# Kernel tuning notes

Hardware: AMD Instinct MI355X
Metric: run time of the kernel (lower is better)

Reference implementation:

```python
import jax, jax.numpy as jnp
import numpy as np

MAX_SEGMENTS = 196
BN_EPS = 1e-5

def _conv(x, w, pad, dil=1):
    return jax.lax.conv_general_dilated(
        x, w, window_strides=(1, 1), padding=[(pad, pad), (pad, pad)],
        rhs_dilation=(dil, dil), dimension_numbers=('NCHW', 'OIHW', 'NCHW'))

def _bn(x, g, b, m, v):
    inv = g / jnp.sqrt(v + BN_EPS)
    return x * inv[None, :, None, None] + (b - m * inv)[None, :, None, None]

def setup_inputs() -> dict:
    key = jax.random.key(0)
    ks = jax.random.split(key, 20)
    B, H, W = 2, 224, 224
    E = 768
    inp = {
        'img': jax.random.normal(ks[0], (B, 3, H, W), jnp.float32),
        'segments': jax.random.randint(ks[1], (B, H, W), 0, MAX_SEGMENTS, jnp.int32),
        'centroids': jax.random.uniform(ks[2], (B, MAX_SEGMENTS, 2), jnp.float32) * 223.0,
        'conv1_w': jax.random.normal(ks[3], (64, 3, 3, 3), jnp.float32) * 0.1,
        'conv1_b': jax.random.normal(ks[4], (64,), jnp.float32) * 0.1,
        'bn1_g': jax.random.uniform(ks[5], (64,), jnp.float32) + 0.5,
        'bn1_b': jax.random.normal(ks[6], (64,), jnp.float32) * 0.1,
        'bn1_m': jax.random.normal(ks[7], (64,), jnp.float32) * 0.1,
        'bn1_v': jax.random.uniform(ks[8], (64,), jnp.float32) + 0.5,
        'conv2_w': jax.random.normal(ks[9], (E, 64, 3, 3), jnp.float32) * 0.05,
        'conv2_b': jax.random.normal(ks[10], (E,), jnp.float32) * 0.1,
        'bn2_g': jax.random.uniform(ks[11], (E,), jnp.float32) + 0.5,
        'bn2_b': jax.random.normal(ks[12], (E,), jnp.float32) * 0.1,
        'bn2_m': jax.random.normal(ks[13], (E,), jnp.float32) * 0.1,
        'bn2_v': jax.random.uniform(ks[14], (E,), jnp.float32) + 0.5,
        'edge_w': jax.random.normal(ks[15], (2, 1, 3, 3), jnp.float32) * 0.2,
        'pos_w': jax.random.normal(ks[16], (E, 2), jnp.float32) * 0.5,
        'pos_b': jax.random.normal(ks[17], (E,), jnp.float32) * 0.1,
        'fusion_w': jax.random.normal(ks[18], (E, 2 * E), jnp.float32) * 0.02,
        'fusion_b': jax.random.normal(ks[19], (E,), jnp.float32) * 0.1,
    }
    return inp

def reference(img, segments, centroids, conv1_w, conv1_b, bn1_g, bn1_b, bn1_m, bn1_v,
              conv2_w, conv2_b, bn2_g, bn2_b, bn2_m, bn2_v, edge_w,
              pos_w, pos_b, fusion_w, fusion_b):
    B, _, H, W = img.shape
    M = MAX_SEGMENTS
    # CNN feature extractor: [B, E, H, W]
    x = jax.nn.relu(_bn(_conv(img, conv1_w, pad=1) + conv1_b[None, :, None, None],
                        bn1_g, bn1_b, bn1_m, bn1_v))
    feats = jax.nn.relu(_bn(_conv(x, conv2_w, pad=2, dil=2) + conv2_b[None, :, None, None],
                            bn2_g, bn2_b, bn2_m, bn2_v))
    C = feats.shape[1]
    # Edge detection on grayscale
    gray = jnp.mean(img, axis=1, keepdims=True)
    edges = _conv(gray, edge_w, pad=1)  # [B, 2, H, W]
    gradient_map = jnp.sqrt(edges[:, 0] ** 2 + edges[:, 1] ** 2 + 1e-8)  # [B, H, W]
    similarity = jnp.clip(1.0 - gradient_map, 0.0, 1.0)
    # Global per-(batch, segment) ids
    ids = (jnp.arange(B, dtype=jnp.int32)[:, None] * M + segments.reshape(B, -1)).reshape(-1)
    K = B * M
    ones = jnp.ones((B * H * W,), jnp.float32)
    counts = jax.ops.segment_sum(ones, ids, num_segments=K)              # [K]
    n_K = jnp.maximum(counts, 1.0)
    sim_sum = jax.ops.segment_sum(similarity.reshape(-1), ids, num_segments=K)
    W_k = (sim_sum / n_K).reshape(B, M)
    # Segment mean / max pooling of features
    ff = feats.transpose(0, 2, 3, 1).reshape(-1, C)                      # [B*H*W, C]
    emb_mean = (jax.ops.segment_sum(ff, ids, num_segments=K) / n_K[:, None]).reshape(B, M, C)
    mx = jax.ops.segment_max(ff, ids, num_segments=K)
    emb_max = jnp.where(counts[:, None] > 0, mx, 0.0).reshape(B, M, C)   # empty segments -> 0
    concat = jnp.concatenate([emb_mean, emb_max], axis=-1)               # [B, M, 2C]
    fused = jnp.einsum('bmc,dc->bmd', concat, fusion_w) + fusion_b
    weighted = fused * W_k[:, :, None]
    # Positional embeddings from normalized centroids
    cn = jnp.stack([centroids[:, :, 0] / float(W), centroids[:, :, 1] / float(H)], axis=-1)
    pos = jnp.einsum('bmc,dc->bmd', cn, pos_w) + pos_b                   # n_centroids == M
    final_embeddings = weighted + pos
    return final_embeddings, gradient_map, segments
```

## Files before the change

kernel.cpp:

```cpp
#include <hip/hip_runtime.h>
#include <hip/hip_fp8.h>

#define B_ 2
#define H_ 224
#define W_ 224
#define HW_ 50176
#define E_ 768
#define M_ 196

typedef __attribute__((ext_vector_type(8))) short short8;
typedef __attribute__((ext_vector_type(8))) unsigned short ushort8;
typedef __attribute__((ext_vector_type(4))) float floatx4;

__device__ __forceinline__ float bf2f(ushort u){ return __uint_as_float(((unsigned)u)<<16); }
__device__ __forceinline__ ushort f2bf(float f){
  unsigned b = __float_as_uint(f);
  b += 0x7fffu + ((b>>16)&1u);
  return (ushort)(b>>16);
}
__device__ __forceinline__ unsigned pack4_fp8(float a, float b, float c, float d){
  int v = __builtin_amdgcn_cvt_pk_fp8_f32(a, b, 0, false);
  v = __builtin_amdgcn_cvt_pk_fp8_f32(c, d, v, true);
  return (unsigned)v;
}

__global__ void prep_edge_k(const float* __restrict__ w2, const float* __restrict__ cb2,
                            const float* __restrict__ g2, const float* __restrict__ be2,
                            const float* __restrict__ mn2, const float* __restrict__ vr2,
                            ushort* __restrict__ wt2, float* __restrict__ bias2,
                            const float* __restrict__ w1, const float* __restrict__ cb1,
                            const float* __restrict__ g1, const float* __restrict__ be1,
                            const float* __restrict__ mn1, const float* __restrict__ vr1,
                            ushort* __restrict__ wA, float* __restrict__ bias1,
                            const float* __restrict__ img, const int* __restrict__ seg,
                            const float* __restrict__ ew, float* __restrict__ out,
                            float* __restrict__ counts, float* __restrict__ sims,
                            int* __restrict__ scnt){
  __shared__ ushort WT[9216];
  __shared__ float aux[196];
  __shared__ float aux2[196];
  int tid = threadIdx.x;
  if (blockIdx.x < 48){
    int co0 = blockIdx.x * 16;
    if (tid < 16){
      float inv = g2[co0+tid] * rsqrtf(vr2[co0+tid] + 1e-5f);
      aux[tid] = inv;
      bias2[co0+tid] = cb2[co0+tid]*inv + be2[co0+tid] - mn2[co0+tid]*inv;
    }
    __syncthreads();
    #pragma unroll
    for (int j = 0; j < 36; j++){
      int idx = j*256 + tid;
      WT[idx] = f2bf(w2[(size_t)co0*576 + idx] * aux[idx/576]);
    }
    __syncthreads();
    #pragma unroll
    for (int j = 0; j < 5; j++){
      int o = j*256 + tid;
      if (o < 1152){
        int tapkc = o >> 4, col = o & 15;
        int tap = tapkc >> 3, kc = tapkc & 7;
        ushort tmp[8];
        #pragma unroll
        for (int e=0; e<8; e++)
          tmp[e] = WT[col*576 + (kc*8+e)*9 + tap];
        *reinterpret_cast<uint4*>(&wt2[(size_t)((tap*8 + kc)*768 + co0 + col)*8]) =
            *reinterpret_cast<const uint4*>(tmp);
      }
    }
    return;
  }
  if (blockIdx.x == 48){
    #pragma unroll
    for (int j = 0; j < 8; j++){
      int t = j*256 + tid;
      int co = t >> 5, k = t & 31;
      float inv = g1[co] * rsqrtf(vr1[co] + 1e-5f);
      float val = 0.f;
      if (k < 27){
        int tap = k / 3, ci = k % 3;
        val = w1[co*27 + ci*9 + tap] * inv;
      }
      wA[co*32 + k] = f2bf(val);
      if (k == 0) bias1[co] = cb1[co]*inv + be1[co] - mn1[co]*inv;
    }
    return;
  }
  if (tid < 196){ aux[tid]=0.f; aux2[tid]=0.f; }
  __syncthreads();
  int p = (blockIdx.x-49)*256 + tid;
  int b = p / HW_; int r = p % HW_; int h = r / W_; int w = r % W_;
  float e0=0.f, e1=0.f;
  #pragma unroll
  for (int ky=0;ky<3;ky++){
    int hh=h+ky-1;
    #pragma unroll
    for (int kx=0;kx<3;kx++){
      int ww=w+kx-1;
      float gv=0.f;
      if (hh>=0&&hh<H_&&ww>=0&&ww<W_){
        int base = b*3*HW_ + hh*W_ + ww;
        gv=(img[base]+img[base+HW_]+img[base+2*HW_])*(1.f/3.f);
      }
      e0 += gv*ew[ky*3+kx];
      e1 += gv*ew[9+ky*3+kx];
    }
  }
  float gm = sqrtf(e0*e0+e1*e1+1e-8f);
  out[301056 + p] = gm;
  int sg = seg[p];
  out[401408 + p] = (float)sg;
  float sim = fminf(fmaxf(1.f-gm,0.f),1.f);
  atomicAdd(&aux[sg], 1.f);
  atomicAdd(&aux2[sg], sim);
  __syncthreads();
  if (tid < 196){
    int gid = b*196 + tid;
    float c = aux[tid];
    atomicAdd(&counts[gid], c);
    atomicAdd(&sims[gid], aux2[tid]);
    atomicAdd(&scnt[b*196+tid], (int)c);
  }
}

__launch_bounds__(256)
__global__ void conv1_scan_k(const float* __restrict__ img, const ushort* __restrict__ wA,
                             const float* __restrict__ bias1, ushort* __restrict__ xbf,
                             const int* __restrict__ scnt, int* __restrict__ offs,
                             int* __restrict__ curs){
  __shared__ float HL[3*18*20];
  __shared__ ushort IC[256*40];
  __shared__ ushort AW[64*40];
  __shared__ float b1s[64];
  int tid = threadIdx.x;
  if (blockIdx.x < 2){
    int* a = reinterpret_cast<int*>(HL);
    int s = blockIdx.x;
    a[tid] = (tid<196)? scnt[s*196+tid] : 0;
    __syncthreads();
    for (int d=1; d<256; d<<=1){
      int v = a[tid];
      int u = (tid>=d)? a[tid-d] : 0;
      __syncthreads();
      a[tid] = v+u;
      __syncthreads();
    }
    if (tid<=196) offs[s*200+tid] = tid ? a[tid-1] : 0;
    if (tid<196)  curs[s*196+tid] = tid ? a[tid-1] : 0;
    return;
  }
  int bid = blockIdx.x - 2;
  int b = bid / 196, tile = bid % 196;
  int tr = tile / 14, tc = tile % 14;
  int h0 = tr*16, w0 = tc*16;
  for (int idx = tid; idx < 972; idx += 256){
    int ci = idx / 324, rem = idx % 324;
    int r = rem / 18, c = rem % 18;
    int hh = h0 + r - 1, ww = w0 + c - 1;
    float v = (hh>=0 && hh<H_ && ww>=0 && ww<W_) ? img[((b*3+ci)*H_+hh)*W_+ww] : 0.f;
    HL[ci*360 + r*20 + c] = v;
  }
  {
    int row = tid >> 2, cp = (tid&3)*8;
    uint4 v = *reinterpret_cast<const uint4*>(&wA[row*32 + cp]);
    *reinterpret_cast<uint4*>(&AW[row*40 + cp]) = v;
  }
  if (tid < 64) b1s[tid] = bias1[tid];
  __syncthreads();
  {
    int pr = tid >> 4, pc = tid & 15;
    ushort tmp[32];
    #pragma unroll
    for (int ky=0; ky<3; ky++)
      #pragma unroll
      for (int kx=0; kx<3; kx++)
        #pragma unroll
        for (int ci=0; ci<3; ci++)
          tmp[(ky*3+kx)*3+ci] = f2bf(HL[ci*360 + (pr+ky)*20 + (pc+kx)]);
    #pragma unroll
    for (int k=27; k<32; k++) tmp[k] = 0;
    #pragma unroll
    for (int j=0; j<4; j++)
      *reinterpret_cast<uint4*>(&IC[tid*40 + j*8]) = *reinterpret_cast<const uint4*>(&tmp[j*8]);
  }
  __syncthreads();
  int lane = tid & 63, wave = tid >> 6;
  int q = lane >> 4, l15 = lane & 15;
  short8 af[4], bfr[4];
  #pragma unroll
  for (int f=0; f<4; f++)
    af[f] = *reinterpret_cast<const short8*>(&AW[(f*16+l15)*40 + q*8]);
  #pragma unroll
  for (int f=0; f<4; f++)
    bfr[f] = *reinterpret_cast<const short8*>(&IC[(wave*64+f*16+l15)*40 + q*8]);
  floatx4 acc[4][4];
  #pragma unroll
  for (int fc=0; fc<4; fc++)
    #pragma unroll
    for (int fp=0; fp<4; fp++){
      floatx4 z = (floatx4){0.f,0.f,0.f,0.f};
      acc[fc][fp] = __builtin_amdgcn_mfma_f32_16x16x32_bf16(af[fc], bfr[fp], z, 0,0,0);
    }
  #pragma unroll
  for (int fp=0; fp<4; fp++){
    int pxl = wave*64 + fp*16 + l15;
    size_t gp = (size_t)b*HW_ + (size_t)(h0 + (pxl>>4))*W_ + (w0 + (pxl&15));
    #pragma unroll
    for (int fc=0; fc<4; fc++){
      int co4 = fc*16 + q*4;
      ushort o[4];
      #pragma unroll
      for (int r=0; r<4; r++) o[r] = f2bf(fmaxf(acc[fc][fp][r] + b1s[co4+r], 0.f));
      *reinterpret_cast<uint2*>(&xbf[gp*64 + co4]) = *reinterpret_cast<const uint2*>(o);
    }
  }
}

__launch_bounds__(256, 2)
__global__ void conv2_scatter_k(const ushort* __restrict__ xbf, const ushort* __restrict__ wt2,
                                const float* __restrict__ bias2, unsigned char* __restrict__ feats,
                                const int* __restrict__ seg, int* __restrict__ curs,
                                int* __restrict__ list){
  __shared__ ushort SM[25600];
  ushort* XH = SM;
  int tid = threadIdx.x;
  if (blockIdx.y == 0){
    if (blockIdx.x < 392){
      int p = blockIdx.x*256 + tid;
      int b = p / HW_;
      int pos = atomicAdd(&curs[b*196+seg[p]], 1);
      list[b*HW_ + pos] = p;
    }
    return;
  }
  int lane = tid & 63, wave = tid >> 6;
  int wc = wave >> 1, wp = wave & 1;
  int q = lane >> 4, l15 = lane & 15;
  int bt = blockIdx.x / 196, tile = blockIdx.x % 196;
  int tr = tile / 14, tc = tile % 14;
  int co0 = (blockIdx.y - 1) * 128;
  int h0 = tr*16, w0 = tc*16;

  for (int px = tid; px < 400; px += 256){
    int hr = px / 20, wcol = px % 20;
    int hh = h0 + hr - 2, ww = w0 + wcol - 2;
    bool ok = (hh>=0 && hh<H_ && ww>=0 && ww<W_);
    const uint4* src = reinterpret_cast<const uint4*>(&xbf[(((size_t)bt*H_+hh)*W_+ww)*64]);
    #pragma unroll
    for (int chl=0; chl<8; chl++){
      uint4 val = ok ? src[chl] : make_uint4(0u,0u,0u,0u);
      *reinterpret_cast<uint4*>(&XH[chl*3200 + px*8]) = val;
    }
  }
  __syncthreads();

  floatx4 acc[4][8];
  #pragma unroll
  for (int i=0;i<4;i++)
    #pragma unroll
    for (int j=0;j<8;j++) acc[i][j] = (floatx4){0.f,0.f,0.f,0.f};

  const int xb = q*3200 + wp*1280 + l15*8;
  const ushort* wgl = wt2 + ((size_t)q*768 + (size_t)(co0 + wc*64 + l15))*8;

  short8 af[2][4], bxA[4], bxB[4];
  #pragma unroll
  for (int f=0; f<4; f++)
    af[0][f] = *reinterpret_cast<const short8*>(&wgl[f*128]);
  #pragma unroll
  for (int fp=0; fp<4; fp++)
    bxA[fp] = *reinterpret_cast<const short8*>(&XH[xb + fp*160]);

  #pragma unroll
  for (int hs = 0; hs < 18; hs++){
    const int cur = hs & 1, nxt = cur ^ 1;
    const int tap = hs >> 1, half = hs & 1;
    const int dyr = (tap/3)*2, dxr = (tap%3)*2;
    const int xoff = half*12800 + dyr*160 + dxr*8;
    if (hs < 17){
      #pragma unroll
      for (int f=0; f<4; f++)
        af[nxt][f] = *reinterpret_cast<const short8*>(&wgl[(size_t)(hs+1)*24576 + f*128]);
    }
    #pragma unroll
    for (int fp=0; fp<4; fp++)
      bxB[fp] = *reinterpret_cast<const short8*>(&XH[xb + xoff + (4+fp)*160]);
    __builtin_amdgcn_sched_barrier(0);
    __builtin_amdgcn_s_setprio(1);
    #pragma unroll
    for (int fc=0; fc<4; fc++)
      #pragma unroll
      for (int fp=0; fp<4; fp++)
        acc[fc][fp] = __builtin_amdgcn_mfma_f32_16x16x32_bf16(af[cur][fc], bxA[fp],
                                                              acc[fc][fp], 0,0,0);
    __builtin_amdgcn_s_setprio(0);
    if (hs < 17){
      const int nh = hs + 1;
      const int ntap = nh >> 1, nhalf = nh & 1;
      const int nxoff = nhalf*12800 + ((ntap/3)*2)*160 + ((ntap%3)*2)*8;
      #pragma unroll
      for (int fp=0; fp<4; fp++)
        bxA[fp] = *reinterpret_cast<const short8*>(&XH[xb + nxoff + fp*160]);
    }
    __builtin_amdgcn_sched_barrier(0);
    __builtin_amdgcn_s_setprio(1);
    #pragma unroll
    for (int fc=0; fc<4; fc++)
      #pragma unroll
      for (int fp=0; fp<4; fp++)
        acc[fc][4+fp] = __builtin_amdgcn_mfma_f32_16x16x32_bf16(af[cur][fc], bxB[fp],
                                                                acc[fc][4+fp], 0,0,0);
    __builtin_amdgcn_s_setprio(0);
  }

  __syncthreads();
  unsigned* EP = reinterpret_cast<unsigned*>(SM);
  #pragma unroll
  for (int fc=0; fc<4; fc++){
    float4 bs = *reinterpret_cast<const float4*>(&bias2[co0 + wc*64 + fc*16 + q*4]);
    int cslot = wc*16 + fc*4 + q;
    #pragma unroll
    for (int fp=0; fp<8; fp++){
      int p_local = (wp*8 + fp)*16 + l15;
      EP[p_local*34 + cslot] = pack4_fp8(
          fmaxf(acc[fc][fp][0] + bs.x, 0.f), fmaxf(acc[fc][fp][1] + bs.y, 0.f),
          fmaxf(acc[fc][fp][2] + bs.z, 0.f), fmaxf(acc[fc][fp][3] + bs.w, 0.f));
    }
  }
  __syncthreads();
  {
    size_t gbase = ((size_t)bt*HW_ + (size_t)(tr*16)*W_ + tc*16)*768 + co0;
    int c = tid & 31, t5 = tid >> 5;
    #pragma unroll
    for (int j=0; j<32; j++){
      int px = j*8 + t5;
      int rr = px >> 4, wcol = px & 15;
      *reinterpret_cast<unsigned*>(
        &feats[gbase + ((size_t)rr*W_ + wcol)*768 + c*4]) = EP[px*34 + c];
    }
  }
}

__global__ void pool_k(const unsigned char* __restrict__ feats, const int* __restrict__ list,
                       const int* __restrict__ offs, float* __restrict__ meansum_p,
                       ushort* __restrict__ maxv_p){
  int m = blockIdx.x, qu = blockIdx.y, b = blockIdx.z, tid = threadIdx.x;
  int base = offs[b*200+m], end = offs[b*200+m+1];
  int len = end - base;
  int b0 = base + ((len*qu) >> 3);
  int b1 = base + ((len*(qu+1)) >> 3);
  const int* lp = &list[b*HW_];
  int co4 = tid*4;
  float s0=0.f,s1=0.f,s2=0.f,s3=0.f;
  float m0=0.f,m1=0.f,m2=0.f,m3=0.f;
  int i = b0;
  #define ACC(v) { \
    float f0=__builtin_amdgcn_cvt_f32_fp8((int)(v),0), f1=__builtin_amdgcn_cvt_f32_fp8((int)(v),1); \
    float f2=__builtin_amdgcn_cvt_f32_fp8((int)(v),2), f3=__builtin_amdgcn_cvt_f32_fp8((int)(v),3); \
    s0+=f0; s1+=f1; s2+=f2; s3+=f3; \
    m0=fmaxf(m0,f0); m1=fmaxf(m1,f1); m2=fmaxf(m2,f2); m3=fmaxf(m3,f3); }
  for (; i+3 < b1; i += 4){
    unsigned va = *reinterpret_cast<const unsigned*>(&feats[(size_t)lp[i  ]*768 + co4]);
    unsigned vb = *reinterpret_cast<const unsigned*>(&feats[(size_t)lp[i+1]*768 + co4]);
    unsigned vc = *reinterpret_cast<const unsigned*>(&feats[(size_t)lp[i+2]*768 + co4]);
    unsigned vd = *reinterpret_cast<const unsigned*>(&feats[(size_t)lp[i+3]*768 + co4]);
    ACC(va) ACC(vb) ACC(vc) ACC(vd)
  }
  for (; i < b1; i++){
    unsigned v = *reinterpret_cast<const unsigned*>(&feats[(size_t)lp[i]*768 + co4]);
    ACC(v)
  }
  #undef ACC
  int gs = b*196 + m;
  size_t slot = ((size_t)qu*392 + gs)*768 + co4;
  *reinterpret_cast<float4*>(&meansum_p[slot]) = make_float4(s0,s1,s2,s3);
  ushort mv[4] = { f2bf(m0), f2bf(m1), f2bf(m2), f2bf(m3) };
  *reinterpret_cast<uint2*>(&maxv_p[slot]) = *reinterpret_cast<const uint2*>(mv);
}

__launch_bounds__(256)
__global__ void fusion_mfma_k(const float* __restrict__ meansum_p, const ushort* __restrict__ maxv_p,
                              const float* __restrict__ counts, const float* __restrict__ fw,
                              float* __restrict__ partial){
  __shared__ ushort SM2[2*128*72];
  ushort* AL = SM2;
  ushort* BL = SM2 + 128*72;
  int tid = threadIdx.x;
  int lane = tid & 63, wave = tid >> 6;
  int wc = wave >> 1, wp = wave & 1;
  int q = lane >> 4, l15 = lane & 15;
  int co0 = blockIdx.x * 128;
  int m0  = blockIdx.y * 128;
  int ksz = blockIdx.z;
  floatx4 acc[4][4];
  for (int i=0;i<4;i++) for (int j=0;j<4;j++) acc[i][j] = (floatx4){0.f,0.f,0.f,0.f};

  for (int kb=0; kb<3; kb++){
    int k0 = ksz*192 + kb*64;
    __syncthreads();
    #pragma unroll
    for (int i=0;i<4;i++){
      int idx = tid + 256*i;
      int row = idx >> 3, c8 = (idx & 7) * 8;
      int gm = m0 + row;
      uint4 aval = make_uint4(0u,0u,0u,0u);
      if (gm < 392){
        int k = k0 + c8;
        if (k < 768){
          float invc = 1.f / fmaxf(counts[gm], 1.f);
          float s[8] = {0.f,0.f,0.f,0.f,0.f,0.f,0.f,0.f};
          #pragma unroll
          for (int qu=0; qu<8; qu++){
            const float4* mp = reinterpret_cast<const float4*>(
                &meansum_p[((size_t)qu*392 + gm)*768 + k]);
            float4 t0 = mp[0], t1 = mp[1];
            s[0]+=t0.x; s[1]+=t0.y; s[2]+=t0.z; s[3]+=t0.w;
            s[4]+=t1.x; s[5]+=t1.y; s[6]+=t1.z; s[7]+=t1.w;
          }
          ushort ua[8];
          #pragma unroll
          for (int e=0; e<8; e++) ua[e] = f2bf(s[e]*invc);
          aval = *reinterpret_cast<const uint4*>(ua);
        } else {
          ushort8 mv = *reinterpret_cast<const ushort8*>(
              &maxv_p[((size_t)gm)*768 + (k-768)]);
          #pragma unroll
          for (int qu=1; qu<8; qu++){
            ushort8 t = *reinterpret_cast<const ushort8*>(
                &maxv_p[((size_t)qu*392 + gm)*768 + (k-768)]);
            mv = __builtin_elementwise_max(mv, t);
          }
          aval = *reinterpret_cast<const uint4*>(&mv);
        }
      }
      *reinterpret_cast<uint4*>(&AL[row*72 + c8]) = aval;
      float4 b0 = *reinterpret_cast<const float4*>(&fw[(co0+row)*1536 + k0 + c8]);
      float4 b1 = *reinterpret_cast<const float4*>(&fw[(co0+row)*1536 + k0 + c8 + 4]);
      ushort ub[8] = { f2bf(b0.x),f2bf(b0.y),f2bf(b0.z),f2bf(b0.w),
                       f2bf(b1.x),f2bf(b1.y),f2bf(b1.z),f2bf(b1.w) };
      *reinterpret_cast<uint4*>(&BL[row*72 + c8]) = *reinterpret_cast<uint4*>(ub);
    }
    __syncthreads();
    #pragma unroll
    for (int ks=0; ks<64; ks+=32){
      short8 af[4], bfr[4];
      #pragma unroll
      for (int f=0; f<4; f++)
        af[f] = *reinterpret_cast<const short8*>(&AL[(wc*64+f*16+l15)*72 + ks + q*8]);
      #pragma unroll
      for (int f=0; f<4; f++)
        bfr[f] = *reinterpret_cast<const short8*>(&BL[(wp*64+f*16+l15)*72 + ks + q*8]);
      #pragma unroll
      for (int fm=0; fm<4; fm++)
        #pragma unroll
        for (int fn=0; fn<4; fn++)
          acc[fm][fn] = __builtin_amdgcn_mfma_f32_16x16x32_bf16(af[fm], bfr[fn], acc[fm][fn], 0,0,0);
    }
  }
  float* pp = &partial[(size_t)ksz * 301056];
  #pragma unroll
  for (int fm=0; fm<4; fm++){
    #pragma unroll
    for (int r2=0; r2<4; r2++){
      int m = m0 + wc*64 + fm*16 + q*4 + r2;
      if (m >= 392) continue;
      #pragma unroll
      for (int fn=0; fn<4; fn++){
        int co = co0 + wp*64 + fn*16 + l15;
        pp[(size_t)m*768 + co] = acc[fm][fn][r2];
      }
    }
  }
}

__global__ void fuse_ep_k(const float* __restrict__ partial, const float* __restrict__ fb,
                          const float* __restrict__ sims, const float* __restrict__ counts,
                          const float* __restrict__ cent, const float* __restrict__ pw,
                          const float* __restrict__ pb, float* __restrict__ out){
  int t = blockIdx.x*256 + threadIdx.x;
  int gm = t / 768, co = t % 768;
  float s = 0.f;
  #pragma unroll
  for (int k=0;k<8;k++) s += partial[(size_t)k*301056 + t];
  float wk = sims[gm] / fmaxf(counts[gm], 1.f);
  float cx = cent[gm*2 + 0] * (1.f/224.f);
  float cy = cent[gm*2 + 1] * (1.f/224.f);
  out[t] = (s + fb[co]) * wk + cx*pw[co*2] + cy*pw[co*2+1] + pb[co];
}

extern "C" void kernel_launch(void* const* d_in, const int* in_sizes, int n_in,
                              void* d_out, int out_size, void* d_ws, size_t ws_size,
                              hipStream_t stream){
  const float* img  = (const float*)d_in[0];
  const int*   seg  = (const int*)  d_in[1];
  const float* cent = (const float*)d_in[2];
  const float* c1w  = (const float*)d_in[3];
  const float* c1b  = (const float*)d_in[4];
  const float* bn1g = (const float*)d_in[5];
  const float* bn1b = (const float*)d_in[6];
  const float* bn1m = (const float*)d_in[7];
  const float* bn1v = (const float*)d_in[8];
  const float* c2w  = (const float*)d_in[9];
  const float* c2b  = (const float*)d_in[10];
  const float* bn2g = (const float*)d_in[11];
  const float* bn2b = (const float*)d_in[12];
  const float* bn2m = (const float*)d_in[13];
  const float* bn2v = (const float*)d_in[14];
  const float* ew   = (const float*)d_in[15];
  const float* pw   = (const float*)d_in[16];
  const float* pb   = (const float*)d_in[17];
  const float* fwp  = (const float*)d_in[18];
  const float* fbp  = (const float*)d_in[19];
  float* out = (float*)d_out;
  char* ws = (char*)d_ws;

  ushort* xbf    = (ushort*)(ws + 0);
  ushort* wt2    = (ushort*)(ws + 12845056);
  float*  bias2  = (float*) (ws + 13729792);
  float*  meansum_p = (float*)(ws + 0);
  ushort* maxv_p    = (ushort*)(ws + 9633792);
  float*  counts = (float*) (ws + 16141312);
  float*  sims   = (float*) (ws + 16142880);
  int*    scnt   = (int*)   (ws + 16144448);
  int*    offs   = (int*)   (ws + 16147584);
  int*    curs   = (int*)   (ws + 16150784);
  int*    list   = (int*)   (ws + 16154112);
  ushort* wA     = (ushort*)(ws + 16154112);
  float*  bias1  = (float*) (ws + 16158208);
  unsigned char* feats = (unsigned char*)(ws + 16555520);
  float*  partial= (float*) (ws + 16555520);

  (void)hipMemsetAsync(ws + 16141312, 0, 6272, stream);
  prep_edge_k<<<441, 256, 0, stream>>>(c2w, c2b, bn2g, bn2b, bn2m, bn2v, wt2, bias2,
                                       c1w, c1b, bn1g, bn1b, bn1m, bn1v, wA, bias1,
                                       img, seg, ew, out, counts, sims, scnt);
  conv1_scan_k<<<394, 256, 0, stream>>>(img, wA, bias1, xbf, scnt, offs, curs);
  conv2_scatter_k<<<dim3(392, 7), 256, 0, stream>>>(xbf, wt2, bias2, feats, seg, curs, list);
  pool_k<<<dim3(196, 8, 2), 192, 0, stream>>>(feats, list, offs, meansum_p, maxv_p);
  fusion_mfma_k<<<dim3(6, 4, 8), 256, 0, stream>>>(meansum_p, maxv_p, counts, fwp, partial);
  fuse_ep_k<<<1176, 256, 0, stream>>>(partial, fbp, sims, counts, cent, pw, pb, out);
}
```

Measured before the change: 260.6 us.

## Tile edge gradient through LDS and hoist partial pool reduction into its own kernel

The edge/gradient part of prep_edge_k now processes 16x16 tiles. Each block loads an 18x18 grayscale halo into shared memory once and computes the 3x3 convolution from LDS, instead of re-reading three image channels nine times per pixel. Separately, a new reduce_pool_k reduces the 8 quarter-partials of mean-sum and max into one bf16 concat matrix. fusion_mfma_k then just loads that matrix, so it no longer repeats the reduction across its 6 column blocks. The cost is one extra kernel launch and an extra round trip through global memory for the concat buffer.

```diff
diff --git a/kernel.cpp b/kernel.cpp
--- a/kernel.cpp
+++ b/kernel.cpp
@@ -86,27 +86,35 @@
     }
     return;
   }
+  float* GR = reinterpret_cast<float*>(WT);
   if (tid < 196){ aux[tid]=0.f; aux2[tid]=0.f; }
-  __syncthreads();
-  int p = (blockIdx.x-49)*256 + tid;
-  int b = p / HW_; int r = p % HW_; int h = r / W_; int w = r % W_;
+  int et = blockIdx.x - 49;
+  int b = et / 196, t196 = et % 196;
+  int tr = t196 / 14, tc = t196 % 14;
+  int h0 = tr*16, w0 = tc*16;
+  for (int i = tid; i < 324; i += 256){
+    int r = i / 18, c = i % 18;
+    int hh = h0 + r - 1, ww = w0 + c - 1;
+    float g = 0.f;
+    if (hh>=0 && hh<H_ && ww>=0 && ww<W_){
+      int base = b*3*HW_ + hh*W_ + ww;
+      g = (img[base] + img[base+HW_] + img[base+2*HW_]) * (1.f/3.f);
+    }
+    GR[i] = g;
+  }
+  __syncthreads();
+  int pr = tid >> 4, pc = tid & 15;
   float e0=0.f, e1=0.f;
   #pragma unroll
-  for (int ky=0;ky<3;ky++){
-    int hh=h+ky-1;
+  for (int ky=0;ky<3;ky++)
     #pragma unroll
     for (int kx=0;kx<3;kx++){
-      int ww=w+kx-1;
-      float gv=0.f;
-      if (hh>=0&&hh<H_&&ww>=0&&ww<W_){
-        int base = b*3*HW_ + hh*W_ + ww;
-        gv=(img[base]+img[base+HW_]+img[base+2*HW_])*(1.f/3.f);
-      }
+      float gv = GR[(pr+ky)*18 + (pc+kx)];
       e0 += gv*ew[ky*3+kx];
       e1 += gv*ew[9+ky*3+kx];
     }
-  }
   float gm = sqrtf(e0*e0+e1*e1+1e-8f);
+  int p = b*HW_ + (h0+pr)*W_ + (w0+pc);
   out[301056 + p] = gm;
   int sg = seg[p];
   out[401408 + p] = (float)sg;
@@ -378,9 +386,42 @@
   *reinterpret_cast<uint2*>(&maxv_p[slot]) = *reinterpret_cast<const uint2*>(mv);
 }
 
+__global__ void reduce_pool_k(const float* __restrict__ meansum_p,
+                              const ushort* __restrict__ maxv_p,
+                              const float* __restrict__ counts,
+                              ushort* __restrict__ cc){
+  int t = blockIdx.x*256 + threadIdx.x;
+  int gm = t / 192;
+  int c8 = (t % 192) * 8;
+  ushort ua[8];
+  if (c8 < 768){
+    float s[8] = {0.f,0.f,0.f,0.f,0.f,0.f,0.f,0.f};
+    #pragma unroll
+    for (int qu=0; qu<8; qu++){
+      const float4* mp = reinterpret_cast<const float4*>(
+          &meansum_p[((size_t)qu*392 + gm)*768 + c8]);
+      float4 t0 = mp[0], t1 = mp[1];
+      s[0]+=t0.x; s[1]+=t0.y; s[2]+=t0.z; s[3]+=t0.w;
+      s[4]+=t1.x; s[5]+=t1.y; s[6]+=t1.z; s[7]+=t1.w;
+    }
+    float invc = 1.f / fmaxf(counts[gm], 1.f);
+    #pragma unroll
+    for (int e=0; e<8; e++) ua[e] = f2bf(s[e]*invc);
+  } else {
+    ushort8 mv = *reinterpret_cast<const ushort8*>(&maxv_p[(size_t)gm*768 + (c8-768)]);
+    #pragma unroll
+    for (int qu=1; qu<8; qu++){
+      ushort8 tt = *reinterpret_cast<const ushort8*>(
+          &maxv_p[((size_t)qu*392 + gm)*768 + (c8-768)]);
+      mv = __builtin_elementwise_max(mv, tt);
+    }
+    *reinterpret_cast<ushort8*>(ua) = mv;
+  }
+  *reinterpret_cast<uint4*>(&cc[(size_t)gm*1536 + c8]) = *reinterpret_cast<const uint4*>(ua);
+}
+
 __launch_bounds__(256)
-__global__ void fusion_mfma_k(const float* __restrict__ meansum_p, const ushort* __restrict__ maxv_p,
-                              const float* __restrict__ counts, const float* __restrict__ fw,
+__global__ void fusion_mfma_k(const ushort* __restrict__ cc, const float* __restrict__ fw,
                               float* __restrict__ partial){
   __shared__ ushort SM2[2*128*72];
   ushort* AL = SM2;
@@ -404,35 +445,8 @@
       int row = idx >> 3, c8 = (idx & 7) * 8;
       int gm = m0 + row;
       uint4 aval = make_uint4(0u,0u,0u,0u);
-      if (gm < 392){
-        int k = k0 + c8;
-        if (k < 768){
-          float invc = 1.f / fmaxf(counts[gm], 1.f);
-          float s[8] = {0.f,0.f,0.f,0.f,0.f,0.f,0.f,0.f};
-          #pragma unroll
-          for (int qu=0; qu<8; qu++){
-            const float4* mp = reinterpret_cast<const float4*>(
-                &meansum_p[((size_t)qu*392 + gm)*768 + k]);
-            float4 t0 = mp[0], t1 = mp[1];
-            s[0]+=t0.x; s[1]+=t0.y; s[2]+=t0.z; s[3]+=t0.w;
-            s[4]+=t1.x; s[5]+=t1.y; s[6]+=t1.z; s[7]+=t1.w;
-          }
-          ushort ua[8];
-          #pragma unroll
-          for (int e=0; e<8; e++) ua[e] = f2bf(s[e]*invc);
-          aval = *reinterpret_cast<const uint4*>(ua);
-        } else {
-          ushort8 mv = *reinterpret_cast<const ushort8*>(
-              &maxv_p[((size_t)gm)*768 + (k-768)]);
-          #pragma unroll
-          for (int qu=1; qu<8; qu++){
-            ushort8 t = *reinterpret_cast<const ushort8*>(
-                &maxv_p[((size_t)qu*392 + gm)*768 + (k-768)]);
-            mv = __builtin_elementwise_max(mv, t);
-          }
-          aval = *reinterpret_cast<const uint4*>(&mv);
-        }
-      }
+      if (gm < 392)
+        aval = *reinterpret_cast<const uint4*>(&cc[(size_t)gm*1536 + k0 + c8]);
       *reinterpret_cast<uint4*>(&AL[row*72 + c8]) = aval;
       float4 b0 = *reinterpret_cast<const float4*>(&fw[(co0+row)*1536 + k0 + c8]);
       float4 b1 = *reinterpret_cast<const float4*>(&fw[(co0+row)*1536 + k0 + c8 + 4]);
@@ -519,6 +533,7 @@
   float*  bias2  = (float*) (ws + 13729792);
   float*  meansum_p = (float*)(ws + 0);
   ushort* maxv_p    = (ushort*)(ws + 9633792);
+  ushort* cc        = (ushort*)(ws + 14450688);
   float*  counts = (float*) (ws + 16141312);
   float*  sims   = (float*) (ws + 16142880);
   int*    scnt   = (int*)   (ws + 16144448);
@@ -537,6 +552,7 @@
   conv1_scan_k<<<394, 256, 0, stream>>>(img, wA, bias1, xbf, scnt, offs, curs);
   conv2_scatter_k<<<dim3(392, 7), 256, 0, stream>>>(xbf, wt2, bias2, feats, seg, curs, list);
   pool_k<<<dim3(196, 8, 2), 192, 0, stream>>>(feats, list, offs, meansum_p, maxv_p);
-  fusion_mfma_k<<<dim3(6, 4, 8), 256, 0, stream>>>(meansum_p, maxv_p, counts, fwp, partial);
+  reduce_pool_k<<<294, 256, 0, stream>>>(meansum_p, maxv_p, counts, cc);
+  fusion_mfma_k<<<dim3(6, 4, 8), 256, 0, stream>>>(cc, fwp, partial);
   fuse_ep_k<<<1176, 256, 0, stream>>>(partial, fbp, sims, counts, cent, pw, pb, out);
 }
```

Result: faster. 253.2 us (-2.9%).
